# Performance work log

Measured on AMD Instinct MI355X. Metric: run time of the kernel, lower is better.

Reference implementation:

```python
import jax, jax.numpy as jnp
import numpy as np

N = 100000        # nodes
E = 1600000       # edges (before self-loops)
IN_CH = 256       # input features
HEADS = 8         # conv1 heads; per-head dim also 8 (GATConv(in, heads, heads=heads))
HID = 8
NCLASS = 64
SLOPE = 0.2       # PyG leaky_relu negative slope


def _gat_conv(x, edge_index, W, att_src, att_dst, bias, heads, ch, concat):
    """PyG GATConv (eval mode): gather -> leaky_relu score -> segment softmax -> scatter."""
    n = x.shape[0]
    src, dst = edge_index[0], edge_index[1]
    h = (x @ W).reshape(n, heads, ch)                      # [N, H, C]
    a_src = jnp.einsum('nhc,hc->nh', h, att_src)           # [N, H]
    a_dst = jnp.einsum('nhc,hc->nh', h, att_dst)
    alpha = jax.nn.leaky_relu(a_src[src] + a_dst[dst], SLOPE)  # [E, H]
    # segment softmax over destination node
    amax = jax.ops.segment_max(alpha, dst, num_segments=n)     # [N, H]
    ex = jnp.exp(alpha - amax[dst])
    denom = jax.ops.segment_sum(ex, dst, num_segments=n)
    coef = ex / (denom[dst] + 1e-16)                           # [E, H]
    out = jax.ops.segment_sum(coef[:, :, None] * h[src], dst, num_segments=n)  # [N, H, C]
    if concat:
        out = out.reshape(n, heads * ch)
    else:
        out = out.mean(axis=1)
    return out + bias


def _add_self_loops(edge_index, n):
    loop = jnp.arange(n, dtype=edge_index.dtype)
    return jnp.concatenate([edge_index, jnp.stack([loop, loop])], axis=1)


def setup_inputs() -> dict:
    key = jax.random.key(0)
    ks = jax.random.split(key, 10)
    g = lambda k, shp, s: (jax.random.normal(k, shp, jnp.float32) * s)
    return {
        'x': jax.random.normal(ks[0], (N, IN_CH), jnp.float32),
        'edge_index': jax.random.randint(ks[1], (2, E), 0, N, dtype=jnp.int64),
        'W1': g(ks[2], (IN_CH, HEADS * HID), 1.0 / np.sqrt(IN_CH)),
        'att_src1': g(ks[3], (HEADS, HID), 0.3),
        'att_dst1': g(ks[4], (HEADS, HID), 0.3),
        'b1': jnp.zeros((HEADS * HID,), jnp.float32),
        'W2': g(ks[5], (HEADS * HID, NCLASS), 1.0 / np.sqrt(HEADS * HID)),
        'att_src2': g(ks[6], (1, NCLASS), 0.3),
        'att_dst2': g(ks[7], (1, NCLASS), 0.3),
        'b2': jnp.zeros((NCLASS,), jnp.float32),
    }


def reference(x, edge_index, W1, att_src1, att_dst1, b1, W2, att_src2, att_dst2, b2):
    ei = _add_self_loops(edge_index, x.shape[0])
    h = jax.nn.elu(_gat_conv(x, ei, W1, att_src1, att_dst1, b1, HEADS, HID, True))
    # dropout is a no-op in eval mode
    h = _gat_conv(h, ei, W2, att_src2, att_dst2, b2, 1, NCLASS, False)
    return jax.nn.log_softmax(h, axis=-1)
```

## Files before the change

kernel.cpp:

```cpp
#include <hip/hip_runtime.h>
#include <hip/hip_bf16.h>

#define LRELU_SLOPE 0.2f
#define NBUK 256
#define BCAP 9728
#define CH2 6144

typedef unsigned int uint;
typedef unsigned short ushort;
typedef short bt8 __attribute__((ext_vector_type(8)));
typedef float fx4 __attribute__((ext_vector_type(4)));

__device__ __forceinline__ ushort f2bf(float f) {
    uint u = __float_as_uint(f);
    return (ushort)((u + 0x7FFF + ((u >> 16) & 1)) >> 16);
}
__device__ __forceinline__ float bf2f(ushort h) {
    return __uint_as_float(((uint)h) << 16);
}

#define ACC8(e, hv) \
    acc[0] += (e) * bf2f((ushort)((hv).x & 0xffff)); \
    acc[1] += (e) * bf2f((ushort)((hv).x >> 16));    \
    acc[2] += (e) * bf2f((ushort)((hv).y & 0xffff)); \
    acc[3] += (e) * bf2f((ushort)((hv).y >> 16));    \
    acc[4] += (e) * bf2f((ushort)((hv).z & 0xffff)); \
    acc[5] += (e) * bf2f((ushort)((hv).z >> 16));    \
    acc[6] += (e) * bf2f((ushort)((hv).w & 0xffff)); \
    acc[7] += (e) * bf2f((ushort)((hv).w >> 16));

__global__ __launch_bounds__(256) void prep_init(
    const float* __restrict__ W1, const float* __restrict__ W2,
    ushort* __restrict__ WT1, ushort* __restrict__ WT2, int* __restrict__ pcur)
{
    int t = threadIdx.x;
    int idx = blockIdx.x * 256 + t;
    if (blockIdx.x == 0) pcur[t] = t * BCAP;
    if (idx < 64 * 256) {
        int c = idx >> 8, k = idx & 255;
        WT1[idx] = f2bf(W1[k * 64 + c]);
    }
    int i2 = idx - 64 * 256;
    if (i2 >= 0 && i2 < 64 * 64) {
        int c = i2 >> 6, k = i2 & 63;
        WT2[i2] = f2bf(W2[k * 64 + c]);
    }
}

__device__ __forceinline__ void partition_body(
    int bid, const int* __restrict__ ei, int E_, int ET,
    int* __restrict__ pcur, uint* __restrict__ pairs,
    int* lcnt, int* lsc, int* lplace, int* gpos)
{
    const int t = threadIdx.x;
    const int base = bid * CH2;
    const int total = min(CH2, ET - base);
    if (total <= 0) return;

    if (t < NBUK) lcnt[t] = 0;
    __syncthreads();

    uint pp[6]; int pk[6];
    #pragma unroll
    for (int i = 0; i < 6; ++i) {
        int idx = t + i * 1024;
        pk[i] = -1;
        if (idx < total) {
            int e = base + idx;
            int s, d;
            if (e < E_) { s = ei[e]; d = ei[E_ + e]; } else { s = d = e - E_; }
            pk[i] = d >> 9;
            pp[i] = (uint)s | ((uint)(d & 511) << 17);
            atomicAdd(&lcnt[pk[i]], 1);
        }
    }
    __syncthreads();

    if (t < NBUK) lsc[t] = lcnt[t];
    __syncthreads();
    for (int off = 1; off < NBUK; off <<= 1) {
        int add = 0;
        if (t < NBUK && t >= off) add = lsc[t - off];
        __syncthreads();
        if (t < NBUK) lsc[t] += add;
        __syncthreads();
    }
    if (t < NBUK) {
        int excl = lsc[t] - lcnt[t];
        lplace[t] = excl;
        int c = lcnt[t];
        gpos[t] = c ? (atomicAdd(&pcur[t], c) - excl) : 0;
    }
    __syncthreads();

    #pragma unroll
    for (int i = 0; i < 6; ++i) {
        if (pk[i] >= 0) {
            int slot = atomicAdd(&lplace[pk[i]], 1);
            pairs[gpos[pk[i]] + slot] = pp[i];
        }
    }
}

__device__ __forceinline__ void gemm1_body4(
    int gbid, const float* __restrict__ X, const ushort* __restrict__ WT,
    ushort* __restrict__ OUT, float* __restrict__ a_src, float* __restrict__ a_dst,
    const float* __restrict__ att_s, const float* __restrict__ att_d, int nrows,
    ushort* wt_l)
{
    constexpr int K = 256, LDW = K + 8, NIT = K / 32;
    const int t = threadIdx.x;
    const int tt = t & 255;
    const int base = (gbid * 4 + (t >> 8)) * 64;

    for (int idx = t * 8; idx < 64 * K; idx += 1024 * 8) {
        int r = idx / K, c = idx % K;
        *(uint4*)&wt_l[r * LDW + c] = *(const uint4*)&WT[idx];
    }
    __syncthreads();

    const int w = tt >> 6, l = tt & 63;
    const int frow = l & 15;
    const int kof = (l >> 4) * 8;
    const int arow = base + 16 * w + frow;
    const bool rowok = arow < nrows;
    const float* xrow = X + (size_t)arow * K + kof;
    fx4 acc[4] = {};

    #pragma unroll
    for (int it = 0; it < NIT; ++it) {
        float4 v0 = make_float4(0.f, 0.f, 0.f, 0.f);
        float4 v1 = make_float4(0.f, 0.f, 0.f, 0.f);
        if (rowok) {
            v0 = *(const float4*)(xrow + it * 32);
            v1 = *(const float4*)(xrow + it * 32 + 4);
        }
        bt8 af;
        af[0] = (short)f2bf(v0.x); af[1] = (short)f2bf(v0.y);
        af[2] = (short)f2bf(v0.z); af[3] = (short)f2bf(v0.w);
        af[4] = (short)f2bf(v1.x); af[5] = (short)f2bf(v1.y);
        af[6] = (short)f2bf(v1.z); af[7] = (short)f2bf(v1.w);
        #pragma unroll
        for (int g = 0; g < 4; ++g) {
            bt8 bf = *(const bt8*)&wt_l[(16 * g + frow) * LDW + it * 32 + kof];
            acc[g] = __builtin_amdgcn_mfma_f32_16x16x32_bf16(af, bf, acc[g], 0, 0, 0);
        }
    }

    const int orow0 = base + 16 * w + (l >> 4) * 4;
    const int ocol = l & 15;
    #pragma unroll
    for (int g = 0; g < 4; ++g) {
        #pragma unroll
        for (int r4 = 0; r4 < 4; ++r4) {
            int gr = orow0 + r4;
            if (gr < nrows) OUT[(size_t)gr * 64 + 16 * g + ocol] = f2bf(acc[g][r4]);
        }
    }

    float as_c[4], ad_c[4];
    #pragma unroll
    for (int g = 0; g < 4; ++g) {
        as_c[g] = att_s[16 * g + ocol];
        ad_c[g] = att_d[16 * g + ocol];
    }
    #pragma unroll
    for (int r4 = 0; r4 < 4; ++r4) {
        int gr = orow0 + r4;
        #pragma unroll
        for (int g = 0; g < 4; ++g) {
            float ps = acc[g][r4] * as_c[g];
            float pd = acc[g][r4] * ad_c[g];
            ps += __shfl_xor(ps, 1, 64); pd += __shfl_xor(pd, 1, 64);
            ps += __shfl_xor(ps, 2, 64); pd += __shfl_xor(pd, 2, 64);
            ps += __shfl_xor(ps, 4, 64); pd += __shfl_xor(pd, 4, 64);
            if ((l & 7) == 0 && gr < nrows) {
                int head = 2 * g + ((l >> 3) & 1);
                a_src[(size_t)gr * 8 + head] = ps;
                a_dst[(size_t)gr * 8 + head] = pd;
            }
        }
    }
}

__global__ __launch_bounds__(1024) void part_gemm1(
    const int* __restrict__ ei, int E_, int ET, int part_grid,
    int* __restrict__ pcur, uint* __restrict__ pairs,
    const float* __restrict__ x, const ushort* __restrict__ WT1,
    ushort* __restrict__ HB, float* __restrict__ a_s1, float* __restrict__ a_d1,
    const float* __restrict__ att_s, const float* __restrict__ att_d, int n)
{
    __shared__ int lcnt[NBUK], lsc[NBUK], lplace[NBUK], gpos[NBUK];
    __shared__ ushort wt_l[64 * 264];
    if ((int)blockIdx.x < part_grid)
        partition_body(blockIdx.x, ei, E_, ET, pcur, pairs, lcnt, lsc, lplace, gpos);
    else
        gemm1_body4(blockIdx.x - part_grid, x, WT1, HB, a_s1, a_d1,
                    att_s, att_d, n, wt_l);
}

__global__ __launch_bounds__(1024) void phase2_build(
    const uint* __restrict__ pairs, const int* __restrict__ pcur,
    int* __restrict__ rp, int* __restrict__ ssrc, int n, int nbuk_used)
{
    __shared__ int hist[512], cur[512], psc[NBUK];
    const int k = blockIdx.x;
    const int t = threadIdx.x;
    const int beg = k * BCAP;
    const int cnt = pcur[k] - beg;
    const int dbase = k << 9;

    if (t < 512) hist[t] = 0;
    if (t < NBUK) psc[t] = (t < nbuk_used) ? (pcur[t] - t * BCAP) : 0;
    __syncthreads();
    for (int off = 1; off < NBUK; off <<= 1) {
        int add = (t < NBUK && t >= off) ? psc[t - off] : 0;
        __syncthreads();
        if (t < NBUK) psc[t] += add;
        __syncthreads();
    }
    const int bbase = k ? psc[k - 1] : 0;

    for (int i = t; i < cnt; i += 1024)
        atomicAdd(&hist[pairs[beg + i] >> 17], 1);
    __syncthreads();

    int c0 = (t < 512) ? hist[t] : 0;
    for (int off = 1; off < 512; off <<= 1) {
        int add = (t < 512 && t >= off) ? hist[t - off] : 0;
        __syncthreads();
        if (t < 512) hist[t] += add;
        __syncthreads();
    }
    if (t < 512) {
        int node = dbase + t;
        if (node < n) rp[node] = bbase + hist[t];
        cur[t] = hist[t] - c0;
    }
    __syncthreads();

    for (int i = t; i < cnt; i += 1024) {
        uint p = pairs[beg + i];
        int j = p >> 17;
        int pos = bbase + atomicAdd(&cur[j], 1);
        ssrc[pos] = (int)(p & 0x1FFFF);
    }
}

__global__ __launch_bounds__(256) void gemm2_att(
    const ushort* __restrict__ X, const ushort* __restrict__ WT,
    ushort* __restrict__ OUT, float* __restrict__ a_src, float* __restrict__ a_dst,
    const float* __restrict__ att_s, const float* __restrict__ att_d, int nrows)
{
    constexpr int K = 64, LDW = K + 8, NIT = K / 32;
    __shared__ ushort wt_l[64 * LDW];
    const int t = threadIdx.x;
    const int base = blockIdx.x * 64;

    for (int idx = t * 8; idx < 64 * K; idx += 256 * 8) {
        int r = idx / K, c = idx % K;
        *(uint4*)&wt_l[r * LDW + c] = *(const uint4*)&WT[idx];
    }
    __syncthreads();

    const int w = t >> 6, l = t & 63;
    const int frow = l & 15;
    const int kof = (l >> 4) * 8;
    const int arow = base + 16 * w + frow;
    const bool rowok = arow < nrows;
    const ushort* xrow = X + (size_t)arow * K + kof;
    fx4 acc[4] = {};

    #pragma unroll
    for (int it = 0; it < NIT; ++it) {
        bt8 af = bt8{0, 0, 0, 0, 0, 0, 0, 0};
        if (rowok) af = *(const bt8*)(xrow + it * 32);
        #pragma unroll
        for (int g = 0; g < 4; ++g) {
            bt8 bf = *(const bt8*)&wt_l[(16 * g + frow) * LDW + it * 32 + kof];
            acc[g] = __builtin_amdgcn_mfma_f32_16x16x32_bf16(af, bf, acc[g], 0, 0, 0);
        }
    }

    const int orow0 = base + 16 * w + (l >> 4) * 4;
    const int ocol = l & 15;
    #pragma unroll
    for (int g = 0; g < 4; ++g) {
        #pragma unroll
        for (int r4 = 0; r4 < 4; ++r4) {
            int gr = orow0 + r4;
            if (gr < nrows) OUT[(size_t)gr * 64 + 16 * g + ocol] = f2bf(acc[g][r4]);
        }
    }

    float as_c[4], ad_c[4];
    #pragma unroll
    for (int g = 0; g < 4; ++g) {
        as_c[g] = att_s[16 * g + ocol];
        ad_c[g] = att_d[16 * g + ocol];
    }
    #pragma unroll
    for (int r4 = 0; r4 < 4; ++r4) {
        int gr = orow0 + r4;
        float ps = 0.f, pd = 0.f;
        #pragma unroll
        for (int g = 0; g < 4; ++g) {
            ps += acc[g][r4] * as_c[g];
            pd += acc[g][r4] * ad_c[g];
        }
        ps += __shfl_xor(ps, 1, 64); pd += __shfl_xor(pd, 1, 64);
        ps += __shfl_xor(ps, 2, 64); pd += __shfl_xor(pd, 2, 64);
        ps += __shfl_xor(ps, 4, 64); pd += __shfl_xor(pd, 4, 64);
        ps += __shfl_xor(ps, 8, 64); pd += __shfl_xor(pd, 8, 64);
        if ((l & 15) == 0 && gr < nrows) {
            a_src[gr] = ps;
            a_dst[gr] = pd;
        }
    }
}

__global__ __launch_bounds__(256) void gather_h8(
    const int* __restrict__ rp, const int* __restrict__ ssrc,
    const float* __restrict__ a_src, const float* __restrict__ a_dst,
    const ushort* __restrict__ HB, const float* __restrict__ bias,
    ushort* __restrict__ HACT, int n)
{
    int node = blockIdx.x * 32 + (threadIdx.x >> 3);
    if (node >= n) return;
    int ol = threadIdx.x & 7;
    int end = rp[node];
    int start = node ? rp[node - 1] : 0;
    float adh = a_dst[(size_t)node * 8 + ol];
    float acc[8] = {};
    float dsum = 0.f;

    int i0 = start;
    for (; i0 + 16 <= end; i0 += 16) {
        int svA = ssrc[i0 + ol];
        int svB = ssrc[i0 + 8 + ol];
        #pragma unroll
        for (int j = 0; j < 8; ++j) {
            int sjA = __shfl(svA, j, 8);
            float aA = a_src[(size_t)sjA * 8 + ol] + adh;
            aA = aA > 0.f ? aA : LRELU_SLOPE * aA;
            float eA = __expf(aA);
            uint4 hvA = *(const uint4*)(HB + (size_t)sjA * 64 + ol * 8);
            dsum += eA; ACC8(eA, hvA);
            int sjB = __shfl(svB, j, 8);
            float aB = a_src[(size_t)sjB * 8 + ol] + adh;
            aB = aB > 0.f ? aB : LRELU_SLOPE * aB;
            float eB = __expf(aB);
            uint4 hvB = *(const uint4*)(HB + (size_t)sjB * 64 + ol * 8);
            dsum += eB; ACC8(eB, hvB);
        }
    }
    for (; i0 < end; i0 += 8) {
        int cnt = min(8, end - i0);
        int sv = (ol < cnt) ? ssrc[i0 + ol] : 0;
        #pragma unroll
        for (int j = 0; j < 8; ++j) {
            int sj = __shfl(sv, j, 8);
            float a = a_src[(size_t)sj * 8 + ol] + adh;
            a = a > 0.f ? a : LRELU_SLOPE * a;
            float e = __expf(a);
            e = (j < cnt) ? e : 0.f;
            uint4 hv = *(const uint4*)(HB + (size_t)sj * 64 + ol * 8);
            dsum += e; ACC8(e, hv);
        }
    }
    float inv = 1.f / (dsum + 1e-16f);
    float4 b0 = *(const float4*)(bias + ol * 8);
    float4 b1 = *(const float4*)(bias + ol * 8 + 4);
    float v[8];
    v[0] = acc[0] * inv + b0.x; v[1] = acc[1] * inv + b0.y;
    v[2] = acc[2] * inv + b0.z; v[3] = acc[3] * inv + b0.w;
    v[4] = acc[4] * inv + b1.x; v[5] = acc[5] * inv + b1.y;
    v[6] = acc[6] * inv + b1.z; v[7] = acc[7] * inv + b1.w;
    #pragma unroll
    for (int c = 0; c < 8; ++c) v[c] = v[c] > 0.f ? v[c] : expm1f(v[c]);
    uint4 o;
    o.x = (uint)f2bf(v[0]) | ((uint)f2bf(v[1]) << 16);
    o.y = (uint)f2bf(v[2]) | ((uint)f2bf(v[3]) << 16);
    o.z = (uint)f2bf(v[4]) | ((uint)f2bf(v[5]) << 16);
    o.w = (uint)f2bf(v[6]) | ((uint)f2bf(v[7]) << 16);
    *(uint4*)(HACT + (size_t)node * 64 + ol * 8) = o;
}

__global__ __launch_bounds__(256) void gather_h1_lsm(
    const int* __restrict__ rp, const int* __restrict__ ssrc,
    const float* __restrict__ a_src, const float* __restrict__ a_dst,
    const ushort* __restrict__ HB, const float* __restrict__ bias,
    float* __restrict__ OUT, int n)
{
    int node = blockIdx.x * 32 + (threadIdx.x >> 3);
    if (node >= n) return;
    int ol = threadIdx.x & 7;
    int end = rp[node];
    int start = node ? rp[node - 1] : 0;
    float ad = a_dst[node];
    float acc[8] = {};
    float dsum = 0.f;

    int i0 = start;
    for (; i0 + 16 <= end; i0 += 16) {
        int svA = ssrc[i0 + ol];
        int svB = ssrc[i0 + 8 + ol];
        #pragma unroll
        for (int j = 0; j < 8; ++j) {
            int sjA = __shfl(svA, j, 8);
            float aA = a_src[sjA] + ad;
            aA = aA > 0.f ? aA : LRELU_SLOPE * aA;
            float eA = __expf(aA);
            uint4 hvA = *(const uint4*)(HB + (size_t)sjA * 64 + ol * 8);
            dsum += eA; ACC8(eA, hvA);
            int sjB = __shfl(svB, j, 8);
            float aB = a_src[sjB] + ad;
            aB = aB > 0.f ? aB : LRELU_SLOPE * aB;
            float eB = __expf(aB);
            uint4 hvB = *(const uint4*)(HB + (size_t)sjB * 64 + ol * 8);
            dsum += eB; ACC8(eB, hvB);
        }
    }
    for (; i0 < end; i0 += 8) {
        int cnt = min(8, end - i0);
        int sv = (ol < cnt) ? ssrc[i0 + ol] : 0;
        #pragma unroll
        for (int j = 0; j < 8; ++j) {
            int sj = __shfl(sv, j, 8);
            float a = a_src[sj] + ad;
            a = a > 0.f ? a : LRELU_SLOPE * a;
            float e = __expf(a);
            e = (j < cnt) ? e : 0.f;
            uint4 hv = *(const uint4*)(HB + (size_t)sj * 64 + ol * 8);
            dsum += e; ACC8(e, hv);
        }
    }
    float inv = 1.f / (dsum + 1e-16f);
    float4 b0 = *(const float4*)(bias + ol * 8);
    float4 b1 = *(const float4*)(bias + ol * 8 + 4);
    float v[8];
    v[0] = acc[0] * inv + b0.x; v[1] = acc[1] * inv + b0.y;
    v[2] = acc[2] * inv + b0.z; v[3] = acc[3] * inv + b0.w;
    v[4] = acc[4] * inv + b1.x; v[5] = acc[5] * inv + b1.y;
    v[6] = acc[6] * inv + b1.z; v[7] = acc[7] * inv + b1.w;

    float m = v[0];
    #pragma unroll
    for (int c = 1; c < 8; ++c) m = fmaxf(m, v[c]);
    m = fmaxf(m, __shfl_xor(m, 1, 8));
    m = fmaxf(m, __shfl_xor(m, 2, 8));
    m = fmaxf(m, __shfl_xor(m, 4, 8));
    float s = 0.f;
    #pragma unroll
    for (int c = 0; c < 8; ++c) s += __expf(v[c] - m);
    s += __shfl_xor(s, 1, 8);
    s += __shfl_xor(s, 2, 8);
    s += __shfl_xor(s, 4, 8);
    float lse = m + __logf(s);
    float4 o0 = make_float4(v[0] - lse, v[1] - lse, v[2] - lse, v[3] - lse);
    float4 o1 = make_float4(v[4] - lse, v[5] - lse, v[6] - lse, v[7] - lse);
    *(float4*)(OUT + (size_t)node * 64 + ol * 8) = o0;
    *(float4*)(OUT + (size_t)node * 64 + ol * 8 + 4) = o1;
}

extern "C" void kernel_launch(void* const* d_in, const int* in_sizes, int n_in,
                              void* d_out, int out_size, void* d_ws, size_t ws_size,
                              hipStream_t stream)
{
    const float* x    = (const float*)d_in[0];
    const int*   ei   = (const int*)d_in[1];
    const float* W1   = (const float*)d_in[2];
    const float* as1w = (const float*)d_in[3];
    const float* ad1w = (const float*)d_in[4];
    const float* b1   = (const float*)d_in[5];
    const float* W2   = (const float*)d_in[6];
    const float* as2w = (const float*)d_in[7];
    const float* ad2w = (const float*)d_in[8];
    const float* b2   = (const float*)d_in[9];
    float* out = (float*)d_out;

    const int n  = in_sizes[0] / 256;
    const int E_ = in_sizes[1] / 2;
    const int ET = E_ + n;
    const int NBUKU = (n + 511) >> 9;

    char* wsb = (char*)d_ws;
    uint*   pairs= (uint*)wsb;
    ushort* HB   = (ushort*)(pairs + (size_t)NBUK*BCAP);
    ushort* HACT = HB + (size_t)n * 64;
    float*  a_s1 = (float*)(HACT + (size_t)n * 64);
    float*  a_d1 = a_s1 + (size_t)n * 8;
    float*  a_s2 = a_d1 + (size_t)n * 8;
    float*  a_d2 = a_s2 + n;
    int*    rp   = (int*)(a_d2 + n);
    int*    pcur = rp + n;
    int*    ssrc = pcur + NBUK;
    ushort* WT1  = (ushort*)(ssrc + ET);
    ushort* WT2  = WT1 + 64 * 256;

    const int gemm_grid  = (n + 63) / 64;
    const int gemm_grid4 = (n + 255) / 256;
    const int gath_grid  = (n + 31) / 32;
    const int part_grid  = (ET + CH2 - 1) / CH2;

    prep_init<<<80, 256, 0, stream>>>(W1, W2, WT1, WT2, pcur);
    part_gemm1<<<part_grid + gemm_grid4, 1024, 0, stream>>>(
        ei, E_, ET, part_grid, pcur, pairs, x, WT1, HB, a_s1, a_d1, as1w, ad1w, n);
    phase2_build<<<NBUKU, 1024, 0, stream>>>(pairs, pcur, rp, ssrc, n, NBUKU);
    gather_h8<<<gath_grid, 256, 0, stream>>>(rp, ssrc, a_s1, a_d1, HB, b1, HACT, n);
    gemm2_att<<<gemm_grid, 256, 0, stream>>>(HACT, WT2, HB, a_s2, a_d2, as2w, ad2w, n);
    gather_h1_lsm<<<gath_grid, 256, 0, stream>>>(rp, ssrc, a_s2, a_d2, HB, b2, out, n);
}
```

Measured before the change: 177.3 us.

## Recompute source attention scores in gathers from loaded features instead of storing them

The gemm kernels no longer compute or store per-node source attention logits. The gather kernels now recompute each edge's source score as a dot product of the already-loaded bf16 feature row with att_src, which removes one dependent random load per edge and the a_src writes. In exchange each edge does extra FMAs, and layer 2 adds three shuffles per edge. The change also software-prefetches the next A fragment in both gemms and puts gemm blocks ahead of partition blocks in the fused launch.

New measurement: 189.0 us. 1.07x slower.

```diff
diff --git a/kernel.cpp b/kernel.cpp
--- a/kernel.cpp
+++ b/kernel.cpp
@@ -19,15 +19,38 @@
     return __uint_as_float(((uint)h) << 16);
 }
 
-#define ACC8(e, hv) \
-    acc[0] += (e) * bf2f((ushort)((hv).x & 0xffff)); \
-    acc[1] += (e) * bf2f((ushort)((hv).x >> 16));    \
-    acc[2] += (e) * bf2f((ushort)((hv).y & 0xffff)); \
-    acc[3] += (e) * bf2f((ushort)((hv).y >> 16));    \
-    acc[4] += (e) * bf2f((ushort)((hv).z & 0xffff)); \
-    acc[5] += (e) * bf2f((ushort)((hv).z >> 16));    \
-    acc[6] += (e) * bf2f((ushort)((hv).w & 0xffff)); \
-    acc[7] += (e) * bf2f((ushort)((hv).w >> 16));
+#define EDGE_H8(sjv, LIVE) { \
+    uint4 hv = *(const uint4*)(HB + (size_t)(sjv) * 64 + ol * 8); \
+    float h0 = bf2f((ushort)(hv.x & 0xffff)), h1 = bf2f((ushort)(hv.x >> 16)); \
+    float h2 = bf2f((ushort)(hv.y & 0xffff)), h3 = bf2f((ushort)(hv.y >> 16)); \
+    float h4 = bf2f((ushort)(hv.z & 0xffff)), h5 = bf2f((ushort)(hv.z >> 16)); \
+    float h6 = bf2f((ushort)(hv.w & 0xffff)), h7 = bf2f((ushort)(hv.w >> 16)); \
+    float dt = h0*w0.x + h1*w0.y + h2*w0.z + h3*w0.w \
+             + h4*w1.x + h5*w1.y + h6*w1.z + h7*w1.w; \
+    float a_ = dt + adh; a_ = a_ > 0.f ? a_ : LRELU_SLOPE * a_; \
+    float e = __expf(a_); \
+    if (!(LIVE)) e = 0.f; \
+    dsum += e; \
+    acc[0] += e*h0; acc[1] += e*h1; acc[2] += e*h2; acc[3] += e*h3; \
+    acc[4] += e*h4; acc[5] += e*h5; acc[6] += e*h6; acc[7] += e*h7; }
+
+#define EDGE_H1(sjv, LIVE) { \
+    uint4 hv = *(const uint4*)(HB + (size_t)(sjv) * 64 + ol * 8); \
+    float h0 = bf2f((ushort)(hv.x & 0xffff)), h1 = bf2f((ushort)(hv.x >> 16)); \
+    float h2 = bf2f((ushort)(hv.y & 0xffff)), h3 = bf2f((ushort)(hv.y >> 16)); \
+    float h4 = bf2f((ushort)(hv.z & 0xffff)), h5 = bf2f((ushort)(hv.z >> 16)); \
+    float h6 = bf2f((ushort)(hv.w & 0xffff)), h7 = bf2f((ushort)(hv.w >> 16)); \
+    float dt = h0*w0.x + h1*w0.y + h2*w0.z + h3*w0.w \
+             + h4*w1.x + h5*w1.y + h6*w1.z + h7*w1.w; \
+    dt += __shfl_xor(dt, 1, 8); \
+    dt += __shfl_xor(dt, 2, 8); \
+    dt += __shfl_xor(dt, 4, 8); \
+    float a_ = dt + ad; a_ = a_ > 0.f ? a_ : LRELU_SLOPE * a_; \
+    float e = __expf(a_); \
+    if (!(LIVE)) e = 0.f; \
+    dsum += e; \
+    acc[0] += e*h0; acc[1] += e*h1; acc[2] += e*h2; acc[3] += e*h3; \
+    acc[4] += e*h4; acc[5] += e*h5; acc[6] += e*h6; acc[7] += e*h7; }
 
 __global__ __launch_bounds__(256) void prep_init(
     const float* __restrict__ W1, const float* __restrict__ W2,
@@ -104,9 +127,8 @@
 
 __device__ __forceinline__ void gemm1_body4(
     int gbid, const float* __restrict__ X, const ushort* __restrict__ WT,
-    ushort* __restrict__ OUT, float* __restrict__ a_src, float* __restrict__ a_dst,
-    const float* __restrict__ att_s, const float* __restrict__ att_d, int nrows,
-    ushort* wt_l)
+    ushort* __restrict__ OUT, float* __restrict__ a_dst,
+    const float* __restrict__ att_d, int nrows, ushort* wt_l)
 {
     constexpr int K = 256, LDW = K + 8, NIT = K / 32;
     const int t = threadIdx.x;
@@ -127,24 +149,28 @@
     const float* xrow = X + (size_t)arow * K + kof;
     fx4 acc[4] = {};
 
+    float4 c0 = make_float4(0.f, 0.f, 0.f, 0.f);
+    float4 c1 = make_float4(0.f, 0.f, 0.f, 0.f);
+    if (rowok) { c0 = *(const float4*)xrow; c1 = *(const float4*)(xrow + 4); }
     #pragma unroll
     for (int it = 0; it < NIT; ++it) {
-        float4 v0 = make_float4(0.f, 0.f, 0.f, 0.f);
-        float4 v1 = make_float4(0.f, 0.f, 0.f, 0.f);
-        if (rowok) {
-            v0 = *(const float4*)(xrow + it * 32);
-            v1 = *(const float4*)(xrow + it * 32 + 4);
+        float4 n0 = make_float4(0.f, 0.f, 0.f, 0.f);
+        float4 n1 = make_float4(0.f, 0.f, 0.f, 0.f);
+        if (it + 1 < NIT && rowok) {
+            n0 = *(const float4*)(xrow + (it + 1) * 32);
+            n1 = *(const float4*)(xrow + (it + 1) * 32 + 4);
         }
         bt8 af;
-        af[0] = (short)f2bf(v0.x); af[1] = (short)f2bf(v0.y);
-        af[2] = (short)f2bf(v0.z); af[3] = (short)f2bf(v0.w);
-        af[4] = (short)f2bf(v1.x); af[5] = (short)f2bf(v1.y);
-        af[6] = (short)f2bf(v1.z); af[7] = (short)f2bf(v1.w);
+        af[0] = (short)f2bf(c0.x); af[1] = (short)f2bf(c0.y);
+        af[2] = (short)f2bf(c0.z); af[3] = (short)f2bf(c0.w);
+        af[4] = (short)f2bf(c1.x); af[5] = (short)f2bf(c1.y);
+        af[6] = (short)f2bf(c1.z); af[7] = (short)f2bf(c1.w);
         #pragma unroll
         for (int g = 0; g < 4; ++g) {
             bt8 bf = *(const bt8*)&wt_l[(16 * g + frow) * LDW + it * 32 + kof];
             acc[g] = __builtin_amdgcn_mfma_f32_16x16x32_bf16(af, bf, acc[g], 0, 0, 0);
         }
+        c0 = n0; c1 = n1;
     }
 
     const int orow0 = base + 16 * w + (l >> 4) * 4;
@@ -158,25 +184,20 @@
         }
     }
 
-    float as_c[4], ad_c[4];
-    #pragma unroll
-    for (int g = 0; g < 4; ++g) {
-        as_c[g] = att_s[16 * g + ocol];
-        ad_c[g] = att_d[16 * g + ocol];
-    }
+    float ad_c[4];
+    #pragma unroll
+    for (int g = 0; g < 4; ++g) ad_c[g] = att_d[16 * g + ocol];
     #pragma unroll
     for (int r4 = 0; r4 < 4; ++r4) {
         int gr = orow0 + r4;
         #pragma unroll
         for (int g = 0; g < 4; ++g) {
-            float ps = acc[g][r4] * as_c[g];
             float pd = acc[g][r4] * ad_c[g];
-            ps += __shfl_xor(ps, 1, 64); pd += __shfl_xor(pd, 1, 64);
-            ps += __shfl_xor(ps, 2, 64); pd += __shfl_xor(pd, 2, 64);
-            ps += __shfl_xor(ps, 4, 64); pd += __shfl_xor(pd, 4, 64);
+            pd += __shfl_xor(pd, 1, 64);
+            pd += __shfl_xor(pd, 2, 64);
+            pd += __shfl_xor(pd, 4, 64);
             if ((l & 7) == 0 && gr < nrows) {
                 int head = 2 * g + ((l >> 3) & 1);
-                a_src[(size_t)gr * 8 + head] = ps;
                 a_dst[(size_t)gr * 8 + head] = pd;
             }
         }
@@ -184,19 +205,19 @@
 }
 
 __global__ __launch_bounds__(1024) void part_gemm1(
-    const int* __restrict__ ei, int E_, int ET, int part_grid,
+    const int* __restrict__ ei, int E_, int ET, int gemm_grid4,
     int* __restrict__ pcur, uint* __restrict__ pairs,
     const float* __restrict__ x, const ushort* __restrict__ WT1,
-    ushort* __restrict__ HB, float* __restrict__ a_s1, float* __restrict__ a_d1,
-    const float* __restrict__ att_s, const float* __restrict__ att_d, int n)
+    ushort* __restrict__ HB, float* __restrict__ a_d1,
+    const float* __restrict__ att_d, int n)
 {
     __shared__ int lcnt[NBUK], lsc[NBUK], lplace[NBUK], gpos[NBUK];
     __shared__ ushort wt_l[64 * 264];
-    if ((int)blockIdx.x < part_grid)
-        partition_body(blockIdx.x, ei, E_, ET, pcur, pairs, lcnt, lsc, lplace, gpos);
+    if ((int)blockIdx.x < gemm_grid4)
+        gemm1_body4(blockIdx.x, x, WT1, HB, a_d1, att_d, n, wt_l);
     else
-        gemm1_body4(blockIdx.x - part_grid, x, WT1, HB, a_s1, a_d1,
-                    att_s, att_d, n, wt_l);
+        partition_body(blockIdx.x - gemm_grid4, ei, E_, ET, pcur, pairs,
+                       lcnt, lsc, lplace, gpos);
 }
 
 __global__ __launch_bounds__(1024) void phase2_build(
@@ -249,8 +270,8 @@
 
 __global__ __launch_bounds__(256) void gemm2_att(
     const ushort* __restrict__ X, const ushort* __restrict__ WT,
-    ushort* __restrict__ OUT, float* __restrict__ a_src, float* __restrict__ a_dst,
-    const float* __restrict__ att_s, const float* __restrict__ att_d, int nrows)
+    ushort* __restrict__ OUT, float* __restrict__ a_dst,
+    const float* __restrict__ att_d, int nrows)
 {
     constexpr int K = 64, LDW = K + 8, NIT = K / 32;
     __shared__ ushort wt_l[64 * LDW];
@@ -271,15 +292,18 @@
     const ushort* xrow = X + (size_t)arow * K + kof;
     fx4 acc[4] = {};
 
+    bt8 cfrag = bt8{0, 0, 0, 0, 0, 0, 0, 0};
+    if (rowok) cfrag = *(const bt8*)xrow;
     #pragma unroll
     for (int it = 0; it < NIT; ++it) {
-        bt8 af = bt8{0, 0, 0, 0, 0, 0, 0, 0};
-        if (rowok) af = *(const bt8*)(xrow + it * 32);
+        bt8 nfrag = bt8{0, 0, 0, 0, 0, 0, 0, 0};
+        if (it + 1 < NIT && rowok) nfrag = *(const bt8*)(xrow + (it + 1) * 32);
         #pragma unroll
         for (int g = 0; g < 4; ++g) {
             bt8 bf = *(const bt8*)&wt_l[(16 * g + frow) * LDW + it * 32 + kof];
-            acc[g] = __builtin_amdgcn_mfma_f32_16x16x32_bf16(af, bf, acc[g], 0, 0, 0);
-        }
+            acc[g] = __builtin_amdgcn_mfma_f32_16x16x32_bf16(cfrag, bf, acc[g], 0, 0, 0);
+        }
+        cfrag = nfrag;
     }
 
     const int orow0 = base + 16 * w + (l >> 4) * 4;
@@ -293,35 +317,26 @@
         }
     }
 
-    float as_c[4], ad_c[4];
-    #pragma unroll
-    for (int g = 0; g < 4; ++g) {
-        as_c[g] = att_s[16 * g + ocol];
-        ad_c[g] = att_d[16 * g + ocol];
-    }
+    float ad_c[4];
+    #pragma unroll
+    for (int g = 0; g < 4; ++g) ad_c[g] = att_d[16 * g + ocol];
     #pragma unroll
     for (int r4 = 0; r4 < 4; ++r4) {
         int gr = orow0 + r4;
-        float ps = 0.f, pd = 0.f;
-        #pragma unroll
-        for (int g = 0; g < 4; ++g) {
-            ps += acc[g][r4] * as_c[g];
-            pd += acc[g][r4] * ad_c[g];
-        }
-        ps += __shfl_xor(ps, 1, 64); pd += __shfl_xor(pd, 1, 64);
-        ps += __shfl_xor(ps, 2, 64); pd += __shfl_xor(pd, 2, 64);
-        ps += __shfl_xor(ps, 4, 64); pd += __shfl_xor(pd, 4, 64);
-        ps += __shfl_xor(ps, 8, 64); pd += __shfl_xor(pd, 8, 64);
-        if ((l & 15) == 0 && gr < nrows) {
-            a_src[gr] = ps;
-            a_dst[gr] = pd;
-        }
+        float pd = 0.f;
+        #pragma unroll
+        for (int g = 0; g < 4; ++g) pd += acc[g][r4] * ad_c[g];
+        pd += __shfl_xor(pd, 1, 64);
+        pd += __shfl_xor(pd, 2, 64);
+        pd += __shfl_xor(pd, 4, 64);
+        pd += __shfl_xor(pd, 8, 64);
+        if ((l & 15) == 0 && gr < nrows) a_dst[gr] = pd;
     }
 }
 
 __global__ __launch_bounds__(256) void gather_h8(
     const int* __restrict__ rp, const int* __restrict__ ssrc,
-    const float* __restrict__ a_src, const float* __restrict__ a_dst,
+    const float* __restrict__ a_dst, const float* __restrict__ att_s,
     const ushort* __restrict__ HB, const float* __restrict__ bias,
     ushort* __restrict__ HACT, int n)
 {
@@ -331,6 +346,8 @@
     int end = rp[node];
     int start = node ? rp[node - 1] : 0;
     float adh = a_dst[(size_t)node * 8 + ol];
+    float4 w0 = *(const float4*)(att_s + ol * 8);
+    float4 w1 = *(const float4*)(att_s + ol * 8 + 4);
     float acc[8] = {};
     float dsum = 0.f;
 
@@ -341,17 +358,9 @@
         #pragma unroll
         for (int j = 0; j < 8; ++j) {
             int sjA = __shfl(svA, j, 8);
-            float aA = a_src[(size_t)sjA * 8 + ol] + adh;
-            aA = aA > 0.f ? aA : LRELU_SLOPE * aA;
-            float eA = __expf(aA);
-            uint4 hvA = *(const uint4*)(HB + (size_t)sjA * 64 + ol * 8);
-            dsum += eA; ACC8(eA, hvA);
+            EDGE_H8(sjA, true);
             int sjB = __shfl(svB, j, 8);
-            float aB = a_src[(size_t)sjB * 8 + ol] + adh;
-            aB = aB > 0.f ? aB : LRELU_SLOPE * aB;
-            float eB = __expf(aB);
-            uint4 hvB = *(const uint4*)(HB + (size_t)sjB * 64 + ol * 8);
-            dsum += eB; ACC8(eB, hvB);
+            EDGE_H8(sjB, true);
         }
     }
     for (; i0 < end; i0 += 8) {
@@ -360,12 +369,7 @@
         #pragma unroll
         for (int j = 0; j < 8; ++j) {
             int sj = __shfl(sv, j, 8);
-            float a = a_src[(size_t)sj * 8 + ol] + adh;
-            a = a > 0.f ? a : LRELU_SLOPE * a;
-            float e = __expf(a);
-            e = (j < cnt) ? e : 0.f;
-            uint4 hv = *(const uint4*)(HB + (size_t)sj * 64 + ol * 8);
-            dsum += e; ACC8(e, hv);
+            EDGE_H8(sj, j < cnt);
         }
     }
     float inv = 1.f / (dsum + 1e-16f);
@@ -388,7 +392,7 @@
 
 __global__ __launch_bounds__(256) void gather_h1_lsm(
     const int* __restrict__ rp, const int* __restrict__ ssrc,
-    const float* __restrict__ a_src, const float* __restrict__ a_dst,
+    const float* __restrict__ a_dst, const float* __restrict__ att_s,
     const ushort* __restrict__ HB, const float* __restrict__ bias,
     float* __restrict__ OUT, int n)
 {
@@ -398,6 +402,8 @@
     int end = rp[node];
     int start = node ? rp[node - 1] : 0;
     float ad = a_dst[node];
+    float4 w0 = *(const float4*)(att_s + ol * 8);
+    float4 w1 = *(const float4*)(att_s + ol * 8 + 4);
     float acc[8] = {};
     float dsum = 0.f;
 
@@ -408,17 +414,9 @@
         #pragma unroll
         for (int j = 0; j < 8; ++j) {
             int sjA = __shfl(svA, j, 8);
-            float aA = a_src[sjA] + ad;
-            aA = aA > 0.f ? aA : LRELU_SLOPE * aA;
-            float eA = __expf(aA);
-            uint4 hvA = *(const uint4*)(HB + (size_t)sjA * 64 + ol * 8);
-            dsum += eA; ACC8(eA, hvA);
+            EDGE_H1(sjA, true);
             int sjB = __shfl(svB, j, 8);
-            float aB = a_src[sjB] + ad;
-            aB = aB > 0.f ? aB : LRELU_SLOPE * aB;
-            float eB = __expf(aB);
-            uint4 hvB = *(const uint4*)(HB + (size_t)sjB * 64 + ol * 8);
-            dsum += eB; ACC8(eB, hvB);
+            EDGE_H1(sjB, true);
         }
     }
     for (; i0 < end; i0 += 8) {
@@ -427,12 +425,7 @@
         #pragma unroll
         for (int j = 0; j < 8; ++j) {
             int sj = __shfl(sv, j, 8);
-            float a = a_src[sj] + ad;
-            a = a > 0.f ? a : LRELU_SLOPE * a;
-            float e = __expf(a);
-            e = (j < cnt) ? e : 0.f;
-            uint4 hv = *(const uint4*)(HB + (size_t)sj * 64 + ol * 8);
-            dsum += e; ACC8(e, hv);
+            EDGE_H1(sj, j < cnt);
         }
     }
     float inv = 1.f / (dsum + 1e-16f);
@@ -488,10 +481,8 @@
     uint*   pairs= (uint*)wsb;
     ushort* HB   = (ushort*)(pairs + (size_t)NBUK*BCAP);
     ushort* HACT = HB + (size_t)n * 64;
-    float*  a_s1 = (float*)(HACT + (size_t)n * 64);
-    float*  a_d1 = a_s1 + (size_t)n * 8;
-    float*  a_s2 = a_d1 + (size_t)n * 8;
-    float*  a_d2 = a_s2 + n;
+    float*  a_d1 = (float*)(HACT + (size_t)n * 64);
+    float*  a_d2 = a_d1 + (size_t)n * 8;
     int*    rp   = (int*)(a_d2 + n);
     int*    pcur = rp + n;
     int*    ssrc = pcur + NBUK;
@@ -504,10 +495,10 @@
     const int part_grid  = (ET + CH2 - 1) / CH2;
 
     prep_init<<<80, 256, 0, stream>>>(W1, W2, WT1, WT2, pcur);
-    part_gemm1<<<part_grid + gemm_grid4, 1024, 0, stream>>>(
-        ei, E_, ET, part_grid, pcur, pairs, x, WT1, HB, a_s1, a_d1, as1w, ad1w, n);
+    part_gemm1<<<gemm_grid4 + part_grid, 1024, 0, stream>>>(
+        ei, E_, ET, gemm_grid4, pcur, pairs, x, WT1, HB, a_d1, ad1w, n);
     phase2_build<<<NBUKU, 1024, 0, stream>>>(pairs, pcur, rp, ssrc, n, NBUKU);
-    gather_h8<<<gath_grid, 256, 0, stream>>>(rp, ssrc, a_s1, a_d1, HB, b1, HACT, n);
-    gemm2_att<<<gemm_grid, 256, 0, stream>>>(HACT, WT2, HB, a_s2, a_d2, as2w, ad2w, n);
-    gather_h1_lsm<<<gath_grid, 256, 0, stream>>>(rp, ssrc, a_s2, a_d2, HB, b2, out, n);
-}
+    gather_h8<<<gath_grid, 256, 0, stream>>>(rp, ssrc, a_d1, as1w, HB, b1, HACT, n);
+    gemm2_att<<<gemm_grid, 256, 0, stream>>>(HACT, WT2, HB, a_d2, ad2w, n);
+    gather_h1_lsm<<<gath_grid, 256, 0, stream>>>(rp, ssrc, a_d2, as2w, HB, b2, out, n);
+}
```
